# Kernel optimization log

Measured on AMD Instinct MI355X. Metric: run time of the kernel, lower is better.

Reference implementation:

```python
import jax, jax.numpy as jnp
import numpy as np

N = 50000   # nodes
E = 800000  # edges
D = 128     # input feature dim
H = 128     # hidden_channels
O = 128     # out_channels
NEG_SLOPE = 0.2


def setup_inputs() -> dict:
    key = jax.random.key(0)
    ks = jax.random.split(key, 16)
    x = jax.random.normal(ks[0], (N, D), dtype=jnp.float32)
    edge_idx = jax.random.randint(ks[1], (2, E), 0, N, dtype=jnp.int32)

    def lin(k, fin, fout):
        return jax.random.normal(k, (fin, fout), dtype=jnp.float32) / np.sqrt(fin)

    params = {
        # layer 1 (D -> H)
        "Wl1": lin(ks[2], D, H), "bl1": jnp.zeros((H,), jnp.float32),
        "Wr1": lin(ks[3], D, H), "br1": jnp.zeros((H,), jnp.float32),
        "att1": jax.random.normal(ks[4], (H,), dtype=jnp.float32) / np.sqrt(H),
        "b1": jnp.zeros((H,), jnp.float32),
        # layer 2 (H -> O)
        "Wl2": lin(ks[5], H, O), "bl2": jnp.zeros((O,), jnp.float32),
        "Wr2": lin(ks[6], H, O), "br2": jnp.zeros((O,), jnp.float32),
        "att2": jax.random.normal(ks[7], (O,), dtype=jnp.float32) / np.sqrt(O),
        "b2": jnp.zeros((O,), jnp.float32),
    }
    return {"x": x, "edge_idx": edge_idx, **params}


def gatv2_layer(x, src, dst, Wl, bl, Wr, br, att, bias):
    """Single-head GATv2Conv (add_self_loops=False), PyG semantics.

    message(x_j) uses lin_l(x_j); score uses leaky_relu(lin_l(x_j)+lin_r(x_i)) @ att,
    softmax over in-edges of each target node, scatter-add weighted messages.
    """
    xl = x @ Wl + bl            # [N, F] source transform
    xr = x @ Wr + br            # [N, F] target transform
    msg = xl[src]               # [E, F] gathered source messages
    e = jax.nn.leaky_relu(msg + xr[dst], NEG_SLOPE)  # [E, F]
    s = e @ att                 # [E] unnormalized scores
    smax = jax.lax.stop_gradient(jax.ops.segment_max(s, dst, num_segments=N))
    p = jnp.exp(s - smax[dst])  # stable segment softmax numerator
    denom = jax.ops.segment_sum(p, dst, num_segments=N)  # [N]
    alpha = p / denom[dst]      # [E]
    out = jax.ops.segment_sum(alpha[:, None] * msg, dst, num_segments=N)
    return out + bias


def reference(x, edge_idx, Wl1, bl1, Wr1, br1, att1, b1, Wl2, bl2, Wr2, br2, att2, b2):
    src, dst = edge_idx[0], edge_idx[1]
    h = jax.nn.relu(gatv2_layer(x, src, dst, Wl1, bl1, Wr1, br1, att1, b1))
    out = gatv2_layer(h, src, dst, Wl2, bl2, Wr2, br2, att2, b2)
    return out
```

## Files before the change

### kernel.cpp

```cpp
#include <hip/hip_runtime.h>
#include <math.h>


typedef short bf16x8 __attribute__((ext_vector_type(8)));
typedef float f32x4 __attribute__((ext_vector_type(4)));

__global__ __launch_bounds__(256) void count_prep_kernel(
    const int* __restrict__ dst, int* __restrict__ deg, int E, int nCnt,
    const float* __restrict__ W0, const float* __restrict__ W1,
    const float* __restrict__ W2, const float* __restrict__ W3,
    short* __restrict__ wt) {
    if ((int)blockIdx.x < nCnt) {
        int i = blockIdx.x * 256 + threadIdx.x;
        if (i < E) atomicAdd(&deg[dst[i]], 1);
    } else {
        int b = blockIdx.x - nCnt;
        int mat = b >> 3, chunk = b & 7;
        const float* W = (mat == 0) ? W0 : (mat == 1) ? W1 : (mat == 2) ? W2 : W3;
        short* hi = wt + (size_t)mat * 2 * 16384;
        short* lo = hi + 16384;
        int i0 = chunk * 2048;
        for (int i = i0 + threadIdx.x; i < i0 + 2048; i += 256) {
            int k = i >> 7, n = i & 127;
            float x = W[i];
            unsigned u = __float_as_uint(x);
            unsigned hu = u & 0xFFFF0000u;
            float lf = x - __uint_as_float(hu);
            hi[n * 128 + k] = (short)(hu >> 16);
            lo[n * 128 + k] = (short)(__float_as_uint(lf) >> 16);
        }
    }
}

__global__ __launch_bounds__(256) void scan_blocksum_kernel(const int* __restrict__ deg,
                                                            int* __restrict__ blockSums, int n) {
    __shared__ int wsum[4];
    int tid = threadIdx.x;
    int idx = blockIdx.x * 256 + tid;
    int v = (idx < n) ? deg[idx] : 0;
    int lane = tid & 63, wid = tid >> 6;
    #pragma unroll
    for (int off = 32; off > 0; off >>= 1) v += __shfl_xor(v, off);
    if (lane == 0) wsum[wid] = v;
    __syncthreads();
    if (tid == 0) blockSums[blockIdx.x] = wsum[0] + wsum[1] + wsum[2] + wsum[3];
}

__global__ __launch_bounds__(256) void scan_apply2_kernel(
    const int* __restrict__ deg, const int* __restrict__ blockSums,
    int* __restrict__ row_ptr, int* __restrict__ writeidx, int n, int nBlk) {
    __shared__ int sPre[4], sAll[4], wsum[4];
    int tid = threadIdx.x, lane = tid & 63, wid = tid >> 6;

    int bsv = (tid < nBlk) ? blockSums[tid] : 0;
    int pre = (tid < (int)blockIdx.x) ? bsv : 0;
    int all = bsv;
    #pragma unroll
    for (int off = 32; off > 0; off >>= 1) {
        pre += __shfl_xor(pre, off);
        all += __shfl_xor(all, off);
    }
    if (lane == 0) { sPre[wid] = pre; sAll[wid] = all; }
    __syncthreads();
    int off0 = sPre[0] + sPre[1] + sPre[2] + sPre[3];
    int total = sAll[0] + sAll[1] + sAll[2] + sAll[3];

    int idx = blockIdx.x * 256 + tid;
    int v = (idx < n) ? deg[idx] : 0;
    int incl = v;
    #pragma unroll
    for (int off = 1; off < 64; off <<= 1) {
        int t = __shfl_up(incl, off);
        if (lane >= off) incl += t;
    }
    if (lane == 63) wsum[wid] = incl;
    __syncthreads();
    int woff = 0;
    #pragma unroll
    for (int w = 0; w < 4; ++w) woff += (w < wid) ? wsum[w] : 0;
    int excl = off0 + woff + (incl - v);
    if (idx < n) { row_ptr[idx] = excl; writeidx[idx] = excl; }
    if (blockIdx.x == 0 && tid == 0) row_ptr[n] = total;
}

__global__ void scatter_edges_kernel(const int* __restrict__ src, const int* __restrict__ dst,
                                     int* __restrict__ writeidx, int* __restrict__ csr_src, int E) {
    int i = blockIdx.x * blockDim.x + threadIdx.x;
    if (i < E) {
        int d = dst[i];
        int pos = atomicAdd(&writeidx[d], 1);
        csr_src[pos] = src[i];
    }
}

#define LDK 136
__global__ __launch_bounds__(256) void gemm_mfma_dual64_kernel(
    const float* __restrict__ X, const short* __restrict__ wtL,
    const float* __restrict__ b0, short* __restrict__ out0bf,
    const float* __restrict__ b1, float* __restrict__ out1,
    int Nrows) {
    __shared__ __attribute__((aligned(16))) short Ahi[64][LDK];
    __shared__ __attribute__((aligned(16))) short Alo[64][LDK];

    int tid = threadIdx.x;
    int w = tid >> 6, lane = tid & 63, q = lane >> 4, tr = lane & 15;
    int m0 = blockIdx.x * 64;
    int n0 = w * 32;

    {
        int srow = tid >> 2;
        int c0 = (tid & 3) * 32;
        int gr = m0 + srow; if (gr >= Nrows) gr = Nrows - 1;
        const float* xp = &X[(size_t)gr * 128 + c0];
        float4 v[8];
        #pragma unroll
        for (int j = 0; j < 8; ++j) v[j] = *(const float4*)(xp + j * 4);
        #pragma unroll
        for (int j = 0; j < 4; ++j) {
            bf16x8 hv, lv;
            #pragma unroll
            for (int k = 0; k < 2; ++k) {
                float4 vv = v[j * 2 + k];
                float f[4] = {vv.x, vv.y, vv.z, vv.w};
                #pragma unroll
                for (int e = 0; e < 4; ++e) {
                    unsigned u = __float_as_uint(f[e]);
                    unsigned hu = u & 0xFFFF0000u;
                    float lf = f[e] - __uint_as_float(hu);
                    hv[k * 4 + e] = (short)(hu >> 16);
                    lv[k * 4 + e] = (short)(__float_as_uint(lf) >> 16);
                }
            }
            *(bf16x8*)&Ahi[srow][c0 + j * 8] = hv;
            *(bf16x8*)&Alo[srow][c0 + j * 8] = lv;
        }
    }
    __syncthreads();

    f32x4 acc[4][4];
    #pragma unroll
    for (int a = 0; a < 4; ++a)
        #pragma unroll
        for (int b = 0; b < 4; ++b) acc[a][b] = (f32x4){0.f, 0.f, 0.f, 0.f};

    for (int kc = 0; kc < 128; kc += 32) {
        bf16x8 bh[4], bl[4];
        #pragma unroll
        for (int p = 0; p < 2; ++p) {
            const short* base = wtL + (size_t)p * 2 * 16384;
            #pragma unroll
            for (int nt = 0; nt < 2; ++nt) {
                size_t boff = (size_t)(n0 + nt * 16 + tr) * 128 + kc + q * 8;
                bh[p * 2 + nt] = *(const bf16x8*)&base[boff];
                bl[p * 2 + nt] = *(const bf16x8*)&base[16384 + boff];
            }
        }
        #pragma unroll
        for (int mt = 0; mt < 4; ++mt) {
            bf16x8 ah = *(const bf16x8*)&Ahi[mt * 16 + tr][kc + q * 8];
            bf16x8 al = *(const bf16x8*)&Alo[mt * 16 + tr][kc + q * 8];
            #pragma unroll
            for (int j = 0; j < 4; ++j) {
                acc[mt][j] = __builtin_amdgcn_mfma_f32_16x16x32_bf16(ah, bh[j], acc[mt][j], 0, 0, 0);
                acc[mt][j] = __builtin_amdgcn_mfma_f32_16x16x32_bf16(ah, bl[j], acc[mt][j], 0, 0, 0);
                acc[mt][j] = __builtin_amdgcn_mfma_f32_16x16x32_bf16(al, bh[j], acc[mt][j], 0, 0, 0);
            }
        }
    }

    #pragma unroll
    for (int nt = 0; nt < 2; ++nt) {
        float bv0 = b0[n0 + nt * 16 + tr];
        float bv1 = b1[n0 + nt * 16 + tr];
        #pragma unroll
        for (int mt = 0; mt < 4; ++mt) {
            #pragma unroll
            for (int r = 0; r < 4; ++r) {
                int row = m0 + mt * 16 + q * 4 + r;
                if (row < Nrows) {
                    float v0 = acc[mt][nt][r] + bv0;
                    unsigned u = __float_as_uint(v0);
                    unsigned rb = (u + 0x7FFFu + ((u >> 16) & 1u)) >> 16;
                    out0bf[(size_t)row * 128 + n0 + nt * 16 + tr] = (short)rb;
                    out1[(size_t)row * 128 + n0 + nt * 16 + tr] = acc[mt][2 + nt][r] + bv1;
                }
            }
        }
    }
}
#undef LDK

__global__ __launch_bounds__(256) void gat_aggregate_kernel(
    const short* __restrict__ xl16, const float* __restrict__ xr,
    const float* __restrict__ att, const float* __restrict__ bias,
    const int* __restrict__ row_ptr, const int* __restrict__ csr_src,
    float* __restrict__ out, int N, int applyRelu) {
    int wid = threadIdx.x >> 6;
    int lane = threadIdx.x & 63;
    int qlane = lane & 15;
    int qid = lane >> 4;
    int node = blockIdx.x * 4 + wid;
    if (node >= N) return;

    const bf16x8* xlb = (const bf16x8*)xl16;
    float4 xrA = ((const float4*)xr)[(size_t)node * 32 + qlane * 2];
    float4 xrB = ((const float4*)xr)[(size_t)node * 32 + qlane * 2 + 1];
    float4 atA = ((const float4*)att)[qlane * 2];
    float4 atB = ((const float4*)att)[qlane * 2 + 1];

    int beg = row_ptr[node];
    int end = row_ptr[node + 1];

    float dsum = 0.f;
    float4 accA = {0.f, 0.f, 0.f, 0.f};
    float4 accB = {0.f, 0.f, 0.f, 0.f};

    for (int cbase = beg; cbase < end; cbase += 64) {
        int cnt = end - cbase;
        if (cnt > 64) cnt = 64;
        int myidx = (lane < cnt) ? csr_src[cbase + lane] : 0;
        int nq = (cnt + 3) >> 2;

        for (int g = 0; g < nq; ++g) {
            int eidx = 4 * g + qid;
            int s = __shfl(myidx, eidx);
            bf16x8 mv = xlb[((size_t)s << 4) + qlane];
            float4 vA, vB;
            vA.x = __uint_as_float(((unsigned)(unsigned short)mv[0]) << 16);
            vA.y = __uint_as_float(((unsigned)(unsigned short)mv[1]) << 16);
            vA.z = __uint_as_float(((unsigned)(unsigned short)mv[2]) << 16);
            vA.w = __uint_as_float(((unsigned)(unsigned short)mv[3]) << 16);
            vB.x = __uint_as_float(((unsigned)(unsigned short)mv[4]) << 16);
            vB.y = __uint_as_float(((unsigned)(unsigned short)mv[5]) << 16);
            vB.z = __uint_as_float(((unsigned)(unsigned short)mv[6]) << 16);
            vB.w = __uint_as_float(((unsigned)(unsigned short)mv[7]) << 16);

            float t, p;
            t = vA.x + xrA.x; t = t > 0.f ? t : 0.2f * t; p = t * atA.x;
            t = vA.y + xrA.y; t = t > 0.f ? t : 0.2f * t; p = fmaf(t, atA.y, p);
            t = vA.z + xrA.z; t = t > 0.f ? t : 0.2f * t; p = fmaf(t, atA.z, p);
            t = vA.w + xrA.w; t = t > 0.f ? t : 0.2f * t; p = fmaf(t, atA.w, p);
            t = vB.x + xrB.x; t = t > 0.f ? t : 0.2f * t; p = fmaf(t, atB.x, p);
            t = vB.y + xrB.y; t = t > 0.f ? t : 0.2f * t; p = fmaf(t, atB.y, p);
            t = vB.z + xrB.z; t = t > 0.f ? t : 0.2f * t; p = fmaf(t, atB.z, p);
            t = vB.w + xrB.w; t = t > 0.f ? t : 0.2f * t; p = fmaf(t, atB.w, p);

            p += __shfl_xor(p, 1);
            p += __shfl_xor(p, 2);
            p += __shfl_xor(p, 4);
            p += __shfl_xor(p, 8);

            float e = (eidx < cnt) ? __expf(p) : 0.f;
            dsum += e;
            accA.x = fmaf(e, vA.x, accA.x);
            accA.y = fmaf(e, vA.y, accA.y);
            accA.z = fmaf(e, vA.z, accA.z);
            accA.w = fmaf(e, vA.w, accA.w);
            accB.x = fmaf(e, vB.x, accB.x);
            accB.y = fmaf(e, vB.y, accB.y);
            accB.z = fmaf(e, vB.z, accB.z);
            accB.w = fmaf(e, vB.w, accB.w);
        }
    }

    #pragma unroll
    for (int off = 16; off <= 32; off <<= 1) {
        dsum += __shfl_xor(dsum, off);
        accA.x += __shfl_xor(accA.x, off);
        accA.y += __shfl_xor(accA.y, off);
        accA.z += __shfl_xor(accA.z, off);
        accA.w += __shfl_xor(accA.w, off);
        accB.x += __shfl_xor(accB.x, off);
        accB.y += __shfl_xor(accB.y, off);
        accB.z += __shfl_xor(accB.z, off);
        accB.w += __shfl_xor(accB.w, off);
    }

    float inv = dsum > 0.f ? 1.f / dsum : 0.f;
    float4 bvA = ((const float4*)bias)[qlane * 2];
    float4 bvB = ((const float4*)bias)[qlane * 2 + 1];
    float4 oA, oB;
    oA.x = accA.x * inv + bvA.x; oA.y = accA.y * inv + bvA.y;
    oA.z = accA.z * inv + bvA.z; oA.w = accA.w * inv + bvA.w;
    oB.x = accB.x * inv + bvB.x; oB.y = accB.y * inv + bvB.y;
    oB.z = accB.z * inv + bvB.z; oB.w = accB.w * inv + bvB.w;
    if (applyRelu) {
        oA.x = fmaxf(oA.x, 0.f); oA.y = fmaxf(oA.y, 0.f);
        oA.z = fmaxf(oA.z, 0.f); oA.w = fmaxf(oA.w, 0.f);
        oB.x = fmaxf(oB.x, 0.f); oB.y = fmaxf(oB.y, 0.f);
        oB.z = fmaxf(oB.z, 0.f); oB.w = fmaxf(oB.w, 0.f);
    }
    if (lane < 16) {
        ((float4*)out)[(size_t)node * 32 + qlane * 2] = oA;
        ((float4*)out)[(size_t)node * 32 + qlane * 2 + 1] = oB;
    }
}


extern "C" void kernel_launch(void* const* d_in, const int* in_sizes, int n_in,
                              void* d_out, int out_size, void* d_ws, size_t ws_size,
                              hipStream_t stream) {
    const float* x    = (const float*)d_in[0];
    const int* eidx   = (const int*)d_in[1];
    const float* Wl1  = (const float*)d_in[2];
    const float* bl1  = (const float*)d_in[3];
    const float* Wr1  = (const float*)d_in[4];
    const float* br1  = (const float*)d_in[5];
    const float* att1 = (const float*)d_in[6];
    const float* b1   = (const float*)d_in[7];
    const float* Wl2  = (const float*)d_in[8];
    const float* bl2  = (const float*)d_in[9];
    const float* Wr2  = (const float*)d_in[10];
    const float* br2  = (const float*)d_in[11];
    const float* att2 = (const float*)d_in[12];
    const float* b2   = (const float*)d_in[13];

    const int N = in_sizes[0] / 128;
    const int E = in_sizes[1] / 2;
    const int* src = eidx;
    const int* dst = eidx + E;

    const int nBlk = (N + 255) / 256;

    size_t NF = (size_t)N * 128;
    short* xl16 = (short*)d_ws;
    float* bufB = (float*)(xl16 + NF);
    float* bufC = bufB + NF;
    int* deg       = (int*)(bufC + NF);
    int* row_ptr   = deg + N;
    int* writeidx  = row_ptr + (N + 1);
    int* csr_src   = writeidx + N;
    int* blockSums = csr_src + E;
    short* wt      = (short*)(blockSums + nBlk);

    float* outF = (float*)d_out;

    const int nCnt = (E + 255) / 256;
    hipMemsetAsync(deg, 0, (size_t)N * sizeof(int), stream);
    count_prep_kernel<<<nCnt + 32, 256, 0, stream>>>(dst, deg, E, nCnt,
                                                     Wl1, Wr1, Wl2, Wr2, wt);
    scan_blocksum_kernel<<<nBlk, 256, 0, stream>>>(deg, blockSums, N);
    scan_apply2_kernel<<<nBlk, 256, 0, stream>>>(deg, blockSums, row_ptr, writeidx, N, nBlk);
    scatter_edges_kernel<<<nCnt, 256, 0, stream>>>(src, dst, writeidx, csr_src, E);

    dim3 gemmGrid((N + 63) / 64);
    dim3 aggGrid((N + 3) / 4);

    gemm_mfma_dual64_kernel<<<gemmGrid, 256, 0, stream>>>(x, wt, bl1, xl16, br1, bufB, N);
    gat_aggregate_kernel<<<aggGrid, 256, 0, stream>>>(xl16, bufB, att1, b1, row_ptr, csr_src,
                                                      bufC, N, 1);
    gemm_mfma_dual64_kernel<<<gemmGrid, 256, 0, stream>>>(bufC, wt + 2 * 2 * 16384, bl2, xl16,
                                                          br2, bufB, N);
    gat_aggregate_kernel<<<aggGrid, 256, 0, stream>>>(xl16, bufB, att2, b2, row_ptr, csr_src,
                                                      outF, N, 0);
}
```

Measured before the change: 337.2 us.

## Record edge ranks during degree count and store CSR sources as 16-bit

The degree-counting atomic now returns each edge's rank within its destination, saved as a 16-bit value. The scatter kernel can then compute each edge's CSR position as row_ptr plus rank, with no second atomic pass and no writeidx buffer. Source indices in the CSR are stored as unsigned 16-bit, which halves the index traffic read by both aggregation kernels. This only works while the node count is below 65536 and every node's in-degree also fits in 16 bits, both of which hold for the fixed problem size.

```diff
diff --git a/kernel.cpp b/kernel.cpp
--- a/kernel.cpp
+++ b/kernel.cpp
@@ -6,13 +6,17 @@
 typedef float f32x4 __attribute__((ext_vector_type(4)));
 
 __global__ __launch_bounds__(256) void count_prep_kernel(
-    const int* __restrict__ dst, int* __restrict__ deg, int E, int nCnt,
+    const int* __restrict__ dst, int* __restrict__ deg,
+    unsigned short* __restrict__ rank16, int E, int nCnt,
     const float* __restrict__ W0, const float* __restrict__ W1,
     const float* __restrict__ W2, const float* __restrict__ W3,
     short* __restrict__ wt) {
     if ((int)blockIdx.x < nCnt) {
         int i = blockIdx.x * 256 + threadIdx.x;
-        if (i < E) atomicAdd(&deg[dst[i]], 1);
+        if (i < E) {
+            int r = atomicAdd(&deg[dst[i]], 1);
+            rank16[i] = (unsigned short)r;
+        }
     } else {
         int b = blockIdx.x - nCnt;
         int mat = b >> 3, chunk = b & 7;
@@ -48,7 +52,7 @@
 
 __global__ __launch_bounds__(256) void scan_apply2_kernel(
     const int* __restrict__ deg, const int* __restrict__ blockSums,
-    int* __restrict__ row_ptr, int* __restrict__ writeidx, int n, int nBlk) {
+    int* __restrict__ row_ptr, int n, int nBlk) {
     __shared__ int sPre[4], sAll[4], wsum[4];
     int tid = threadIdx.x, lane = tid & 63, wid = tid >> 6;
 
@@ -79,17 +83,19 @@
     #pragma unroll
     for (int w = 0; w < 4; ++w) woff += (w < wid) ? wsum[w] : 0;
     int excl = off0 + woff + (incl - v);
-    if (idx < n) { row_ptr[idx] = excl; writeidx[idx] = excl; }
+    if (idx < n) row_ptr[idx] = excl;
     if (blockIdx.x == 0 && tid == 0) row_ptr[n] = total;
 }
 
 __global__ void scatter_edges_kernel(const int* __restrict__ src, const int* __restrict__ dst,
-                                     int* __restrict__ writeidx, int* __restrict__ csr_src, int E) {
+                                     const int* __restrict__ row_ptr,
+                                     const unsigned short* __restrict__ rank16,
+                                     unsigned short* __restrict__ csr16, int E) {
     int i = blockIdx.x * blockDim.x + threadIdx.x;
     if (i < E) {
         int d = dst[i];
-        int pos = atomicAdd(&writeidx[d], 1);
-        csr_src[pos] = src[i];
+        int pos = row_ptr[d] + (int)rank16[i];
+        csr16[pos] = (unsigned short)src[i];
     }
 }
 
@@ -193,7 +199,7 @@
 __global__ __launch_bounds__(256) void gat_aggregate_kernel(
     const short* __restrict__ xl16, const float* __restrict__ xr,
     const float* __restrict__ att, const float* __restrict__ bias,
-    const int* __restrict__ row_ptr, const int* __restrict__ csr_src,
+    const int* __restrict__ row_ptr, const unsigned short* __restrict__ csr16,
     float* __restrict__ out, int N, int applyRelu) {
     int wid = threadIdx.x >> 6;
     int lane = threadIdx.x & 63;
@@ -218,7 +224,7 @@
     for (int cbase = beg; cbase < end; cbase += 64) {
         int cnt = end - cbase;
         if (cnt > 64) cnt = 64;
-        int myidx = (lane < cnt) ? csr_src[cbase + lane] : 0;
+        int myidx = (lane < cnt) ? (int)csr16[cbase + lane] : 0;
         int nq = (cnt + 3) >> 2;
 
         for (int g = 0; g < nq; ++g) {
@@ -328,29 +334,29 @@
     float* bufC = bufB + NF;
     int* deg       = (int*)(bufC + NF);
     int* row_ptr   = deg + N;
-    int* writeidx  = row_ptr + (N + 1);
-    int* csr_src   = writeidx + N;
-    int* blockSums = csr_src + E;
-    short* wt      = (short*)(blockSums + nBlk);
+    int* blockSums = row_ptr + (N + 1);
+    unsigned short* rank16 = (unsigned short*)(blockSums + nBlk);
+    unsigned short* csr16  = rank16 + E;
+    short* wt      = (short*)(csr16 + E);
 
     float* outF = (float*)d_out;
 
     const int nCnt = (E + 255) / 256;
     hipMemsetAsync(deg, 0, (size_t)N * sizeof(int), stream);
-    count_prep_kernel<<<nCnt + 32, 256, 0, stream>>>(dst, deg, E, nCnt,
+    count_prep_kernel<<<nCnt + 32, 256, 0, stream>>>(dst, deg, rank16, E, nCnt,
                                                      Wl1, Wr1, Wl2, Wr2, wt);
     scan_blocksum_kernel<<<nBlk, 256, 0, stream>>>(deg, blockSums, N);
-    scan_apply2_kernel<<<nBlk, 256, 0, stream>>>(deg, blockSums, row_ptr, writeidx, N, nBlk);
-    scatter_edges_kernel<<<nCnt, 256, 0, stream>>>(src, dst, writeidx, csr_src, E);
+    scan_apply2_kernel<<<nBlk, 256, 0, stream>>>(deg, blockSums, row_ptr, N, nBlk);
+    scatter_edges_kernel<<<nCnt, 256, 0, stream>>>(src, dst, row_ptr, rank16, csr16, E);
 
     dim3 gemmGrid((N + 63) / 64);
     dim3 aggGrid((N + 3) / 4);
 
     gemm_mfma_dual64_kernel<<<gemmGrid, 256, 0, stream>>>(x, wt, bl1, xl16, br1, bufB, N);
-    gat_aggregate_kernel<<<aggGrid, 256, 0, stream>>>(xl16, bufB, att1, b1, row_ptr, csr_src,
+    gat_aggregate_kernel<<<aggGrid, 256, 0, stream>>>(xl16, bufB, att1, b1, row_ptr, csr16,
                                                       bufC, N, 1);
     gemm_mfma_dual64_kernel<<<gemmGrid, 256, 0, stream>>>(bufC, wt + 2 * 2 * 16384, bl2, xl16,
                                                           br2, bufB, N);
-    gat_aggregate_kernel<<<aggGrid, 256, 0, stream>>>(xl16, bufB, att2, b2, row_ptr, csr_src,
+    gat_aggregate_kernel<<<aggGrid, 256, 0, stream>>>(xl16, bufB, att2, b2, row_ptr, csr16,
                                                       outF, N, 0);
 }
```

After: 295.5 us. 12.4% less time.
